# Kernel optimization log

Measured on AMD Instinct MI355X. Metric: run time of the kernel, lower is better.

## Reference

```python
import jax, jax.numpy as jnp
import numpy as np

HEADS, DH = 8, 64  # SelfAttention defaults: heads=8, dim_head=64


def _layernorm(x, g, b, eps=1e-5):
    mu = x.mean(-1, keepdims=True)
    var = ((x - mu) ** 2).mean(-1, keepdims=True)
    return (x - mu) / jnp.sqrt(var + eps) * g + b


def setup_inputs() -> dict:
    key = jax.random.key(0)
    ks = jax.random.split(key, 13)
    B, H, W, D, P = 1, 256, 256, 64, 128
    inner = HEADS * DH
    s = 0.05  # weight scale to keep logits in a sane range
    return {
        "x": jax.random.normal(ks[0], (B, H, W, D), jnp.float32),
        "pair_bias": jax.random.normal(ks[1], (B, W, W, P), jnp.float32),
        "Wq_w": jax.random.normal(ks[2], (D, inner), jnp.float32) * s,
        "Wkv_w": jax.random.normal(ks[3], (D, 2 * inner), jnp.float32) * s,
        "Wout_w": jax.random.normal(ks[4], (inner, D), jnp.float32) * s,
        "bout_w": jnp.zeros((D,), jnp.float32),
        "Wq_h": jax.random.normal(ks[5], (D, inner), jnp.float32) * s,
        "Wkv_h": jax.random.normal(ks[6], (D, 2 * inner), jnp.float32) * s,
        "Wout_h": jax.random.normal(ks[7], (inner, D), jnp.float32) * s,
        "bout_h": jnp.zeros((D,), jnp.float32),
        "pair_ln_g": jnp.ones((P,), jnp.float32),
        "pair_ln_b": jnp.zeros((P,), jnp.float32),
        "W_pair": jax.random.normal(ks[8], (P, HEADS), jnp.float32) * s,
    }


def _qkv(x2d, Wq, Wkv):
    # x2d: (N, L, D) -> q, k, v each (N, heads, L, dh)
    N, L, _ = x2d.shape
    q = (x2d @ Wq).reshape(N, L, HEADS, DH).transpose(0, 2, 1, 3)
    kv = (x2d @ Wkv).reshape(N, L, 2, HEADS, DH)
    k = kv[:, :, 0].transpose(0, 2, 1, 3)
    v = kv[:, :, 1].transpose(0, 2, 1, 3)
    return q, k, v


def reference(x, pair_bias, Wq_w, Wkv_w, Wout_w, bout_w,
              Wq_h, Wkv_h, Wout_h, bout_h, pair_ln_g, pair_ln_b, W_pair):
    B, H, W, D = x.shape  # B=1, H=n_seqs, W=length, D=dim
    scale = DH ** -0.5

    # ---- width attention: attend over seq dim H, batched per column (b*w) ----
    xw = jnp.transpose(x, (0, 2, 1, 3)).reshape(B * W, H, D)
    q, k, v = _qkv(xw, Wq_w, Wkv_w)
    dots = jnp.einsum('bhid,bhjd->bhij', q, k) * scale  # (B*W, heads, H, H)
    attn = jax.nn.softmax(dots, axis=-1)
    ow = jnp.einsum('bhij,bhjd->bhid', attn, v)
    ow = ow.transpose(0, 2, 1, 3).reshape(B * W, H, HEADS * DH)
    ow = ow @ Wout_w + bout_w
    w_out = ow.reshape(B, W, H, D).transpose(0, 2, 1, 3)  # (B, H, W, D)

    # ---- height attention: tied over seq dim (tie_attn_dim=H), pair bias ----
    xh = x.reshape(B * H, W, D)
    q, k, v = _qkv(xh, Wq_h, Wkv_h)           # (B*H, heads, W, dh)
    q = q.reshape(B, H, HEADS, W, DH)
    k = k.reshape(B, H, HEADS, W, DH)
    v = v.reshape(B, H, HEADS, W, DH)
    dots = jnp.einsum('brhid,brhjd->bhij', q, k) * scale * (H ** -0.5)  # (B, heads, W, W)
    pb = _layernorm(pair_bias, pair_ln_g, pair_ln_b) @ W_pair  # (B, W, W, heads)
    dots = dots + pb.transpose(0, 3, 1, 2)
    attn = jax.nn.softmax(dots, axis=-1)
    oh = jnp.einsum('bhij,brhjd->brhid', attn, v)  # (B, H, heads, W, dh)
    oh = oh.transpose(0, 1, 3, 2, 4).reshape(B, H, W, HEADS * DH)
    h_out = oh @ Wout_h + bout_h  # (B, H, W, D)

    return (w_out + h_out) * 0.5
```

## Files before the change

### kernel.cpp

```cpp
#include <hip/hip_runtime.h>
#include <hip/hip_bf16.h>

typedef __hip_bfloat16 bf16;
typedef __attribute__((ext_vector_type(8))) short bf16x8;
typedef __attribute__((ext_vector_type(4))) float f32x4;

#define MFMA16(a, b, c) __builtin_amdgcn_mfma_f32_16x16x32_bf16(a, b, c, 0, 0, 0)

#define HH 256
#define WW 256
#define NHEADS 8
#define NROWS 65536


__device__ __forceinline__ bf16x8 cvt8(const float* f) {
  bf16x8 r;
  bf16* h = (bf16*)&r;
#pragma unroll
  for (int i = 0; i < 8; i++) h[i] = __float2bfloat16(f[i]);
  return r;
}

__global__ void __launch_bounds__(256) k_xT2(const float* __restrict__ x,
                                             bf16* __restrict__ xh,
                                             bf16* __restrict__ xw) {
  const size_t idx = ((size_t)blockIdx.x * 256 + threadIdx.x) * 4;
  const float4 v = *(const float4*)(x + idx);
  bf16 tmp[4];
  tmp[0] = __float2bfloat16(v.x);
  tmp[1] = __float2bfloat16(v.y);
  tmp[2] = __float2bfloat16(v.z);
  tmp[3] = __float2bfloat16(v.w);
  *(uint2*)(xh + idx) = *(const uint2*)tmp;
  const int n = (int)(idx >> 6), d = (int)(idx & 63);
  const int h = n >> 8, w = n & 255;
  *(uint2*)(xw + (((size_t)((w << 8) | h)) << 6) + d) = *(const uint2*)tmp;
}

__global__ void __launch_bounds__(256) k_wt2(const float* __restrict__ Wq_w,
                                             const float* __restrict__ Wkv_w,
                                             const float* __restrict__ Wq_h,
                                             const float* __restrict__ Wkv_h,
                                             bf16* __restrict__ Wt_w,
                                             bf16* __restrict__ Wt_h) {
  int idx = blockIdx.x * 256 + threadIdx.x;
  const float* Wq = Wq_w;
  const float* Wkv = Wkv_w;
  bf16* Wt = Wt_w;
  if (idx >= 98304) { idx -= 98304; Wq = Wq_h; Wkv = Wkv_h; Wt = Wt_h; }
  const int k = idx / 1536, c = idx - k * 1536;
  const float val = (c < 512) ? Wq[k * 512 + c] : Wkv[k * 1024 + (c - 512)];
  Wt[(size_t)c * 64 + k] = __float2bfloat16(val);
}

__global__ void __launch_bounds__(256) k_wo(const float* __restrict__ Wout_w,
                                            const float* __restrict__ Wout_h,
                                            bf16* __restrict__ Wo_w,
                                            bf16* __restrict__ Wo_h) {
  int idx = blockIdx.x * 256 + threadIdx.x;
  const float* W = Wout_w;
  bf16* dst = Wo_w;
  if (idx >= 32768) { idx -= 32768; W = Wout_h; dst = Wo_h; }
  const int c = idx >> 9, d = idx & 511;
  dst[idx] = __float2bfloat16(W[d * 64 + c]);
}

__global__ void __launch_bounds__(256, 2)
k_width_fused(const bf16* __restrict__ xw, const bf16* __restrict__ Wt,
              bf16* __restrict__ Ow) {
  __shared__ __align__(16) char smem[53248];
  bf16* Ks = (bf16*)(smem + 20480);
  bf16* Vt = (bf16*)(smem + 36864);
  const int w = blockIdx.x, head = blockIdx.y;
  const int tid = threadIdx.x, lane = tid & 63, wv = tid >> 6;
  bf16* Qsc = (bf16*)(smem + wv * 5120);
  bf16* Ps  = (bf16*)(smem + wv * 5120);
  const int m16 = lane & 15, kq = lane >> 4;
  const int i0 = wv * 64;
  const bf16* xcol = xw + (size_t)w * 256 * 64;

  bf16x8 qf[4][2];
#pragma unroll
  for (int ch = 0; ch < 2; ch++) {
    bf16x8 af[2][2];
#pragma unroll
    for (int mt = 0; mt < 2; mt++) {
      const bf16* xr = xcol + (size_t)(i0 + ch * 32 + mt * 16 + m16) * 64 + kq * 8;
      af[mt][0] = *(const bf16x8*)xr;
      af[mt][1] = *(const bf16x8*)(xr + 32);
    }
#pragma unroll
    for (int nt = 0; nt < 4; nt++) {
      const bf16* wp = Wt + (size_t)(head * 64 + nt * 16 + m16) * 64 + kq * 8;
      const bf16x8 w0 = *(const bf16x8*)wp;
      const bf16x8 w1 = *(const bf16x8*)(wp + 32);
#pragma unroll
      for (int mt = 0; mt < 2; mt++) {
        f32x4 a = (f32x4){0.f, 0.f, 0.f, 0.f};
        a = MFMA16(af[mt][0], w0, a);
        a = MFMA16(af[mt][1], w1, a);
#pragma unroll
        for (int r = 0; r < 4; r++) {
          const int li = mt * 16 + kq * 4 + r;
          const int d = nt * 16 + m16;
          Qsc[li * 64 + (((d >> 3) ^ (li & 7)) << 3) + (d & 7)] = __float2bfloat16(a[r]);
        }
      }
    }
#pragma unroll
    for (int it = 0; it < 2; it++)
#pragma unroll
      for (int ks = 0; ks < 2; ks++) {
        const int li = it * 16 + m16;
        qf[ch * 2 + it][ks] =
            *(const bf16x8*)&Qsc[li * 64 + (((ks * 4 + kq) ^ (li & 7)) << 3)];
      }
  }

  f32x4 acc[4][4];
#pragma unroll
  for (int a = 0; a < 4; a++)
#pragma unroll
    for (int b = 0; b < 4; b++) acc[a][b] = (f32x4){0.f, 0.f, 0.f, 0.f};
  float rsum[4][4];
#pragma unroll
  for (int a = 0; a < 4; a++)
#pragma unroll
    for (int r = 0; r < 4; r++) rsum[a][r] = 0.f;

#pragma unroll 1
  for (int half = 0; half < 2; half++) {
    if (half) __syncthreads();
    bf16x8 afk[2][2];
#pragma unroll
    for (int mt = 0; mt < 2; mt++) {
      const int jrow = half * 128 + wv * 32 + mt * 16 + m16;
      const bf16* xr = xcol + (size_t)jrow * 64 + kq * 8;
      afk[mt][0] = *(const bf16x8*)xr;
      afk[mt][1] = *(const bf16x8*)(xr + 32);
    }
#pragma unroll
    for (int nt = 0; nt < 4; nt++) {
      const int d = nt * 16 + m16;
      {
        const bf16* wp = Wt + (size_t)(512 + head * 64 + d) * 64 + kq * 8;
        const bf16x8 w0 = *(const bf16x8*)wp;
        const bf16x8 w1 = *(const bf16x8*)(wp + 32);
#pragma unroll
        for (int mt = 0; mt < 2; mt++) {
          f32x4 a = (f32x4){0.f, 0.f, 0.f, 0.f};
          a = MFMA16(afk[mt][0], w0, a);
          a = MFMA16(afk[mt][1], w1, a);
#pragma unroll
          for (int r = 0; r < 4; r++) {
            const int jl = wv * 32 + mt * 16 + kq * 4 + r;
            Ks[jl * 64 + (((d >> 3) ^ (jl & 7)) << 3) + (d & 7)] = __float2bfloat16(a[r]);
          }
        }
      }
      {
        const bf16* wp = Wt + (size_t)(1024 + head * 64 + d) * 64 + kq * 8;
        const bf16x8 w0 = *(const bf16x8*)wp;
        const bf16x8 w1 = *(const bf16x8*)(wp + 32);
#pragma unroll
        for (int mt = 0; mt < 2; mt++) {
          f32x4 a = (f32x4){0.f, 0.f, 0.f, 0.f};
          a = MFMA16(afk[mt][0], w0, a);
          a = MFMA16(afk[mt][1], w1, a);
          const int jb = wv * 32 + mt * 16 + kq * 4;
          bf16 tmp[4];
#pragma unroll
          for (int r = 0; r < 4; r++) tmp[r] = __float2bfloat16(a[r]);
          *(uint2*)&Vt[d * 128 + (((jb >> 3) ^ (d & 7)) << 3) + (jb & 7)] =
              *(const uint2*)tmp;
        }
      }
    }
    __syncthreads();
#pragma unroll 1
    for (int jcl = 0; jcl < 4; jcl++) {
      bf16x8 kf[2][2];
#pragma unroll
      for (int jt = 0; jt < 2; jt++) {
        const int j = jcl * 32 + jt * 16 + m16;
#pragma unroll
        for (int ks = 0; ks < 2; ks++)
          kf[jt][ks] = *(const bf16x8*)&Ks[j * 64 + (((ks * 4 + kq) ^ (j & 7)) << 3)];
      }
#pragma unroll
      for (int it = 0; it < 4; it++)
#pragma unroll
        for (int jt = 0; jt < 2; jt++) {
          f32x4 s = (f32x4){0.f, 0.f, 0.f, 0.f};
          s = MFMA16(qf[it][0], kf[jt][0], s);
          s = MFMA16(qf[it][1], kf[jt][1], s);
#pragma unroll
          for (int r = 0; r < 4; r++) {
            float p = __expf(s[r] * 0.125f);
            rsum[it][r] += p;
            Ps[(it * 16 + kq * 4 + r) * 40 + jt * 16 + m16] = __float2bfloat16(p);
          }
        }
      bf16x8 pf[4], vf[4];
#pragma unroll
      for (int it = 0; it < 4; it++)
        pf[it] = *(const bf16x8*)&Ps[(it * 16 + m16) * 40 + kq * 8];
#pragma unroll
      for (int dt = 0; dt < 4; dt++)
        vf[dt] = *(const bf16x8*)&Vt[(dt * 16 + m16) * 128 +
                                     (((jcl * 4 + kq) ^ (m16 & 7)) << 3)];
#pragma unroll
      for (int it = 0; it < 4; it++)
#pragma unroll
        for (int dt = 0; dt < 4; dt++) acc[it][dt] = MFMA16(pf[it], vf[dt], acc[it][dt]);
    }
  }

#pragma unroll
  for (int it = 0; it < 4; it++)
#pragma unroll
    for (int r = 0; r < 4; r++) {
      float s = rsum[it][r];
      s += __shfl_xor(s, 1); s += __shfl_xor(s, 2);
      s += __shfl_xor(s, 4); s += __shfl_xor(s, 8);
      rsum[it][r] = 1.f / s;
    }
#pragma unroll
  for (int it = 0; it < 4; it++)
#pragma unroll
    for (int dt = 0; dt < 4; dt++)
#pragma unroll
      for (int r = 0; r < 4; r++) {
        const int i = i0 + it * 16 + kq * 4 + r;
        Ow[((size_t)(w * 256 + i)) * 512 + head * 64 + dt * 16 + m16] =
            __float2bfloat16(acc[it][dt][r] * rsum[it][r]);
      }
}

__global__ void __launch_bounds__(256, 2)
k_dots_f(const bf16* __restrict__ xh, const bf16* __restrict__ Wt, float* __restrict__ dp) {
  __shared__ __align__(16) bf16 Qs[64 * 72];
  __shared__ __align__(16) bf16 Ks[64 * 72];
  const int tile = blockIdx.x, head = blockIdx.y, rc = blockIdx.z;
  const int i0 = (tile >> 2) * 64, j0 = (tile & 3) * 64;
  const int tid = threadIdx.x, lane = tid & 63, wv = tid >> 6;
  const int m16 = lane & 15, kq = lane >> 4;
  float* slice = dp + (size_t)rc * 524288 + (size_t)head * 65536;

  const bf16* WtQ = Wt + (size_t)(head * 64) * 64 + kq * 8;
  const bf16* WtK = Wt + (size_t)(512 + head * 64) * 64 + kq * 8;

  f32x4 acc[4];
#pragma unroll
  for (int b = 0; b < 4; b++) acc[b] = (f32x4){0.f, 0.f, 0.f, 0.f};

  const int lrow = wv * 16 + kq * 4;

#pragma unroll 1
  for (int rr = 0; rr < 32; rr++) {
    const int rbase = (rc * 32 + rr) * 256;
    __syncthreads();
    {
      const bf16* xr = xh + (size_t)(rbase + i0 + wv * 16 + m16) * 64 + kq * 8;
      const bf16x8 qa0 = *(const bf16x8*)xr;
      const bf16x8 qa1 = *(const bf16x8*)(xr + 32);
      const bf16* yr = xh + (size_t)(rbase + j0 + wv * 16 + m16) * 64 + kq * 8;
      const bf16x8 ka0 = *(const bf16x8*)yr;
      const bf16x8 ka1 = *(const bf16x8*)(yr + 32);
#pragma unroll
      for (int nt = 0; nt < 4; nt++) {
        const bf16* wq = WtQ + (size_t)(nt * 16 + m16) * 64;
        f32x4 aq = (f32x4){0.f, 0.f, 0.f, 0.f};
        aq = MFMA16(qa0, *(const bf16x8*)wq, aq);
        aq = MFMA16(qa1, *(const bf16x8*)(wq + 32), aq);
        const bf16* wk = WtK + (size_t)(nt * 16 + m16) * 64;
        f32x4 ak = (f32x4){0.f, 0.f, 0.f, 0.f};
        ak = MFMA16(ka0, *(const bf16x8*)wk, ak);
        ak = MFMA16(ka1, *(const bf16x8*)(wk + 32), ak);
#pragma unroll
        for (int r = 0; r < 4; r++) {
          Qs[(lrow + r) * 72 + nt * 16 + m16] = __float2bfloat16(aq[r]);
          Ks[(lrow + r) * 72 + nt * 16 + m16] = __float2bfloat16(ak[r]);
        }
      }
    }
    __syncthreads();
#pragma unroll
    for (int ks = 0; ks < 2; ks++) {
      bf16x8 af = *(const bf16x8*)&Qs[(wv * 16 + m16) * 72 + ks * 32 + kq * 8];
      bf16x8 bfr[4];
#pragma unroll
      for (int jt = 0; jt < 4; jt++)
        bfr[jt] = *(const bf16x8*)&Ks[(jt * 16 + m16) * 72 + ks * 32 + kq * 8];
#pragma unroll
      for (int jt = 0; jt < 4; jt++) acc[jt] = MFMA16(af, bfr[jt], acc[jt]);
    }
  }
  const float sc = 1.f / 128.f;
#pragma unroll
  for (int jt = 0; jt < 4; jt++)
#pragma unroll
    for (int r = 0; r < 4; r++)
      slice[(size_t)(i0 + wv * 16 + kq * 4 + r) * 256 + j0 + jt * 16 + m16] = acc[jt][r] * sc;
}

__global__ void __launch_bounds__(256) k_pb(const float* __restrict__ pb,
                                            const float* __restrict__ g,
                                            const float* __restrict__ bb,
                                            const float* __restrict__ Wp,
                                            float* __restrict__ dots) {
  __shared__ float sn[4][128];
  const int tid = threadIdx.x, lane = tid & 63, wv = tid >> 6;
  const size_t ij = (size_t)blockIdx.x * 4 + wv;
  const float2 xv = *(const float2*)(pb + ij * 128 + lane * 2);

  float s = xv.x + xv.y;
#pragma unroll
  for (int o = 1; o < 64; o <<= 1) s += __shfl_xor(s, o);
  const float mu = s * (1.f / 128.f);
  const float d0 = xv.x - mu, d1 = xv.y - mu;
  float s2 = d0 * d0 + d1 * d1;
#pragma unroll
  for (int o = 1; o < 64; o <<= 1) s2 += __shfl_xor(s2, o);
  const float inv = rsqrtf(s2 * (1.f / 128.f) + 1e-5f);

  sn[wv][lane * 2 + 0] = d0 * inv * g[lane * 2 + 0] + bb[lane * 2 + 0];
  sn[wv][lane * 2 + 1] = d1 * inv * g[lane * 2 + 1] + bb[lane * 2 + 1];

  const int h = lane & 7, gp = lane >> 3;
  float a = 0.f;
#pragma unroll
  for (int p0 = 0; p0 < 16; p0++) {
    const int p = gp * 16 + p0;
    a += sn[wv][p] * Wp[p * 8 + h];
  }
  a += __shfl_xor(a, 8);
  a += __shfl_xor(a, 16);
  a += __shfl_xor(a, 32);
  if (lane < 8) dots[(size_t)h * 65536 + ij] += a;
}

__global__ void __launch_bounds__(256) k_softmax8(const float* __restrict__ dp,
                                                  bf16* __restrict__ P) {
  __shared__ float red[4];
  const int i = blockIdx.x, head = blockIdx.y, t = threadIdx.x;
  const size_t base = (size_t)head * 65536 + i * 256 + t;
  float lg = 0.f;
#pragma unroll
  for (int s = 0; s < 8; s++) lg += dp[(size_t)s * 524288 + base];
  const float e = __expf(lg);
  float s = e;
#pragma unroll
  for (int o = 1; o < 64; o <<= 1) s += __shfl_xor(s, o);
  if ((t & 63) == 0) red[t >> 6] = s;
  __syncthreads();
  const float S = red[0] + red[1] + red[2] + red[3];
  P[base] = __float2bfloat16(e / S);
}

__global__ void __launch_bounds__(256, 2)
k_h_pv_f(const bf16* __restrict__ P, const bf16* __restrict__ xh,
         const bf16* __restrict__ Wt, bf16* __restrict__ Oh) {
  __shared__ __align__(16) bf16 Vt[64 * 256];
  const int r = blockIdx.x, head = blockIdx.y;
  const int tid = threadIdx.x, lane = tid & 63, wv = tid >> 6;
  const int m16 = lane & 15, kq = lane >> 4;

  {
    const bf16* WtV = Wt + (size_t)(1024 + head * 64) * 64 + kq * 8;
#pragma unroll
    for (int mt = 0; mt < 4; mt++) {
      const int jb16 = wv * 64 + mt * 16;
      const bf16* xr = xh + (size_t)(r * 256 + jb16 + m16) * 64 + kq * 8;
      const bf16x8 a0 = *(const bf16x8*)xr;
      const bf16x8 a1 = *(const bf16x8*)(xr + 32);
#pragma unroll
      for (int nt = 0; nt < 4; nt++) {
        const int d = nt * 16 + m16;
        const bf16* wp = WtV + (size_t)(nt * 16 + m16) * 64;
        f32x4 a = (f32x4){0.f, 0.f, 0.f, 0.f};
        a = MFMA16(a0, *(const bf16x8*)wp, a);
        a = MFMA16(a1, *(const bf16x8*)(wp + 32), a);
        const int j = jb16 + kq * 4;
        bf16 tmp[4];
#pragma unroll
        for (int r2 = 0; r2 < 4; r2++) tmp[r2] = __float2bfloat16(a[r2]);
        *(uint2*)&Vt[d * 256 + (((j >> 3) ^ (d & 7)) << 3) + (j & 7)] = *(const uint2*)tmp;
      }
    }
  }

  const bf16* Pb = P + (size_t)head * 65536;
  const int i0 = wv * 64;
  auto loadP = [&](int ks, bf16x8 pf[4]) {
#pragma unroll
    for (int it = 0; it < 4; it++)
      pf[it] = *(const bf16x8*)(Pb + (size_t)(i0 + it * 16 + m16) * 256 + ks * 32 + kq * 8);
  };
  bf16x8 pcur[4];
  loadP(0, pcur);
  __syncthreads();

  f32x4 acc[4][4];
#pragma unroll
  for (int a = 0; a < 4; a++)
#pragma unroll
    for (int b = 0; b < 4; b++) acc[a][b] = (f32x4){0.f, 0.f, 0.f, 0.f};

#pragma unroll 1
  for (int ks = 0; ks < 8; ks++) {
    bf16x8 pnext[4];
    if (ks < 7) loadP(ks + 1, pnext);
    bf16x8 vf[4];
#pragma unroll
    for (int dt = 0; dt < 4; dt++)
      vf[dt] = *(const bf16x8*)&Vt[(dt * 16 + m16) * 256 + (((ks * 4 + kq) ^ (m16 & 7)) << 3)];
#pragma unroll
    for (int it = 0; it < 4; it++)
#pragma unroll
      for (int dt = 0; dt < 4; dt++) acc[it][dt] = MFMA16(pcur[it], vf[dt], acc[it][dt]);
    if (ks < 7) {
#pragma unroll
      for (int it = 0; it < 4; it++) pcur[it] = pnext[it];
    }
  }
#pragma unroll
  for (int it = 0; it < 4; it++)
#pragma unroll
    for (int dt = 0; dt < 4; dt++)
#pragma unroll
      for (int r2 = 0; r2 < 4; r2++) {
        const int i = i0 + it * 16 + kq * 4 + r2;
        Oh[((size_t)(r * 256 + i)) * 512 + head * 64 + dt * 16 + m16] =
            __float2bfloat16(acc[it][dt][r2]);
      }
}

__global__ void __launch_bounds__(256) k_outproj(const bf16* __restrict__ Ow,
                                                 const bf16* __restrict__ Oh,
                                                 const bf16* __restrict__ Wow,
                                                 const bf16* __restrict__ Woh,
                                                 const float* __restrict__ bw,
                                                 const float* __restrict__ bh,
                                                 float* __restrict__ out) {
  const int tid = threadIdx.x, lane = tid & 63, wv = tid >> 6;
  const int m16 = lane & 15, kq = lane >> 4;
  const int nA = blockIdx.x * 64 + wv * 16 + m16;
  const int wA = ((nA & 255) << 8) | (nA >> 8);

  const bf16* aw = Ow + (size_t)wA * 512 + kq * 8;
  const bf16* ah = Oh + (size_t)nA * 512 + kq * 8;

  f32x4 acc[4];
#pragma unroll
  for (int ct = 0; ct < 4; ct++) acc[ct] = (f32x4){0.f, 0.f, 0.f, 0.f};

#pragma unroll 1
  for (int kc = 0; kc < 16; kc++) {
    const bf16x8 afw = *(const bf16x8*)(aw + kc * 32);
    const bf16x8 afh = *(const bf16x8*)(ah + kc * 32);
#pragma unroll
    for (int ct = 0; ct < 4; ct++) {
      const bf16x8 bfw = *(const bf16x8*)(Wow + (size_t)(ct * 16 + m16) * 512 + kc * 32 + kq * 8);
      const bf16x8 bfh = *(const bf16x8*)(Woh + (size_t)(ct * 16 + m16) * 512 + kc * 32 + kq * 8);
      acc[ct] = MFMA16(afw, bfw, acc[ct]);
      acc[ct] = MFMA16(afh, bfh, acc[ct]);
    }
  }
  const int n0 = blockIdx.x * 64 + wv * 16 + kq * 4;
#pragma unroll
  for (int ct = 0; ct < 4; ct++) {
    const int c = ct * 16 + m16;
    const float bias = 0.5f * (bw[c] + bh[c]);
#pragma unroll
    for (int r = 0; r < 4; r++)
      out[(size_t)(n0 + r) * 64 + c] = 0.5f * acc[ct][r] + bias;
  }
}

extern "C" void kernel_launch(void* const* d_in, const int* in_sizes, int n_in,
                              void* d_out, int out_size, void* d_ws, size_t ws_size,
                              hipStream_t stream) {
  const float* x      = (const float*)d_in[0];
  const float* pair   = (const float*)d_in[1];
  const float* Wq_w   = (const float*)d_in[2];
  const float* Wkv_w  = (const float*)d_in[3];
  const float* Wout_w = (const float*)d_in[4];
  const float* bout_w = (const float*)d_in[5];
  const float* Wq_h   = (const float*)d_in[6];
  const float* Wkv_h  = (const float*)d_in[7];
  const float* Wout_h = (const float*)d_in[8];
  const float* bout_h = (const float*)d_in[9];
  const float* ln_g   = (const float*)d_in[10];
  const float* ln_b   = (const float*)d_in[11];
  const float* W_pair = (const float*)d_in[12];
  float* out = (float*)d_out;

  char* ws = (char*)d_ws;
  bf16* R0 = (bf16*)ws;
  bf16* xh = (bf16*)(ws + 67108864);
  bf16* xw = (bf16*)(ws + 67108864 + 8388608);
  bf16* R2 = (bf16*)(ws + 134217728);
  bf16* Wt_w = (bf16*)(ws + 201326592);
  bf16* Wt_h = (bf16*)(ws + 201326592 + 393216);
  bf16* P  = (bf16*)(ws + 201326592 + 786432);
  bf16* Wo_w = (bf16*)(ws + 201326592 + 1835008);
  bf16* Wo_h = Wo_w + 32768;
  float* dp = out;

  k_xT2<<<4096, 256, 0, stream>>>(x, xh, xw);
  k_wt2<<<768, 256, 0, stream>>>(Wq_w, Wkv_w, Wq_h, Wkv_h, Wt_w, Wt_h);
  k_wo<<<256, 256, 0, stream>>>(Wout_w, Wout_h, Wo_w, Wo_h);

  k_width_fused<<<dim3(WW, NHEADS), 256, 0, stream>>>(xw, Wt_w, R0);

  k_dots_f<<<dim3(16, NHEADS, 8), 256, 0, stream>>>(xh, Wt_h, dp);
  k_pb<<<65536 / 4, 256, 0, stream>>>(pair, ln_g, ln_b, W_pair, dp);
  k_softmax8<<<dim3(256, NHEADS), 256, 0, stream>>>(dp, P);
  k_h_pv_f<<<dim3(HH, NHEADS), 256, 0, stream>>>(P, xh, Wt_h, R2);

  k_outproj<<<1024, 256, 0, stream>>>(R0, R2, Wo_w, Wo_h, bout_w, bout_h, out);
}
```

Before: 447.1 us.

## Fold Q and K projections into per-head 64x64 bilinear matrix

Precomputes M = Wq_head · Wk_headᵀ for each head in a small kernel. Scores are then computed as (x·M)·xᵀ instead of projecting both Q and K. This removes the K projection and its shared-memory staging in both the width and height attention score kernels, and k_dots_f no longer needs block-wide barriers. In exchange, a second bf16 rounding of the fused matrix may change precision, and K fragments are now read directly from global memory.

```diff
diff --git a/kernel.cpp b/kernel.cpp
--- a/kernel.cpp
+++ b/kernel.cpp
@@ -65,12 +65,42 @@
   dst[idx] = __float2bfloat16(W[d * 64 + c]);
 }
 
+__global__ void __launch_bounds__(256) k_mb(const float* __restrict__ Wq_w,
+                                            const float* __restrict__ Wkv_w,
+                                            const float* __restrict__ Wq_h,
+                                            const float* __restrict__ Wkv_h,
+                                            bf16* __restrict__ Mb) {
+  __shared__ float Aq[64][64];
+  __shared__ float Ak[64][64];
+  const int phase = blockIdx.x >> 3, head = blockIdx.x & 7;
+  const float* Wq = phase ? Wq_h : Wq_w;
+  const float* Wkv = phase ? Wkv_h : Wkv_w;
+  const int t = threadIdx.x;
+#pragma unroll
+  for (int i = 0; i < 16; i++) {
+    const int idx = i * 256 + t;
+    const int r = idx >> 6, c = idx & 63;
+    Aq[r][c] = Wq[r * 512 + head * 64 + c];
+    Ak[r][c] = Wkv[r * 1024 + head * 64 + c];
+  }
+  __syncthreads();
+  bf16* dst = Mb + ((size_t)(phase * 8 + head)) * 4096;
+#pragma unroll
+  for (int i = 0; i < 16; i++) {
+    const int idx = i * 256 + t;
+    const int d2 = idx >> 6, d1 = idx & 63;
+    float s = 0.f;
+#pragma unroll
+    for (int dh = 0; dh < 64; dh++) s += Aq[d1][dh] * Ak[d2][dh];
+    dst[idx] = __float2bfloat16(s);
+  }
+}
+
 __global__ void __launch_bounds__(256, 2)
 k_width_fused(const bf16* __restrict__ xw, const bf16* __restrict__ Wt,
-              bf16* __restrict__ Ow) {
-  __shared__ __align__(16) char smem[53248];
-  bf16* Ks = (bf16*)(smem + 20480);
-  bf16* Vt = (bf16*)(smem + 36864);
+              const bf16* __restrict__ Mb, bf16* __restrict__ Ow) {
+  __shared__ __align__(16) char smem[36864];
+  bf16* Vt = (bf16*)(smem + 20480);
   const int w = blockIdx.x, head = blockIdx.y;
   const int tid = threadIdx.x, lane = tid & 63, wv = tid >> 6;
   bf16* Qsc = (bf16*)(smem + wv * 5120);
@@ -78,8 +108,9 @@
   const int m16 = lane & 15, kq = lane >> 4;
   const int i0 = wv * 64;
   const bf16* xcol = xw + (size_t)w * 256 * 64;
-
-  bf16x8 qf[4][2];
+  const bf16* Mh = Mb + (size_t)head * 4096;
+
+  bf16x8 yf[4][2];
 #pragma unroll
   for (int ch = 0; ch < 2; ch++) {
     bf16x8 af[2][2];
@@ -91,7 +122,7 @@
     }
 #pragma unroll
     for (int nt = 0; nt < 4; nt++) {
-      const bf16* wp = Wt + (size_t)(head * 64 + nt * 16 + m16) * 64 + kq * 8;
+      const bf16* wp = Mh + (size_t)(nt * 16 + m16) * 64 + kq * 8;
       const bf16x8 w0 = *(const bf16x8*)wp;
       const bf16x8 w1 = *(const bf16x8*)(wp + 32);
 #pragma unroll
@@ -112,7 +143,7 @@
 #pragma unroll
       for (int ks = 0; ks < 2; ks++) {
         const int li = it * 16 + m16;
-        qf[ch * 2 + it][ks] =
+        yf[ch * 2 + it][ks] =
             *(const bf16x8*)&Qsc[li * 64 + (((ks * 4 + kq) ^ (li & 7)) << 3)];
       }
   }
@@ -142,38 +173,20 @@
 #pragma unroll
     for (int nt = 0; nt < 4; nt++) {
       const int d = nt * 16 + m16;
-      {
-        const bf16* wp = Wt + (size_t)(512 + head * 64 + d) * 64 + kq * 8;
-        const bf16x8 w0 = *(const bf16x8*)wp;
-        const bf16x8 w1 = *(const bf16x8*)(wp + 32);
-#pragma unroll
-        for (int mt = 0; mt < 2; mt++) {
-          f32x4 a = (f32x4){0.f, 0.f, 0.f, 0.f};
-          a = MFMA16(afk[mt][0], w0, a);
-          a = MFMA16(afk[mt][1], w1, a);
-#pragma unroll
-          for (int r = 0; r < 4; r++) {
-            const int jl = wv * 32 + mt * 16 + kq * 4 + r;
-            Ks[jl * 64 + (((d >> 3) ^ (jl & 7)) << 3) + (d & 7)] = __float2bfloat16(a[r]);
-          }
-        }
-      }
-      {
-        const bf16* wp = Wt + (size_t)(1024 + head * 64 + d) * 64 + kq * 8;
-        const bf16x8 w0 = *(const bf16x8*)wp;
-        const bf16x8 w1 = *(const bf16x8*)(wp + 32);
-#pragma unroll
-        for (int mt = 0; mt < 2; mt++) {
-          f32x4 a = (f32x4){0.f, 0.f, 0.f, 0.f};
-          a = MFMA16(afk[mt][0], w0, a);
-          a = MFMA16(afk[mt][1], w1, a);
-          const int jb = wv * 32 + mt * 16 + kq * 4;
-          bf16 tmp[4];
-#pragma unroll
-          for (int r = 0; r < 4; r++) tmp[r] = __float2bfloat16(a[r]);
-          *(uint2*)&Vt[d * 128 + (((jb >> 3) ^ (d & 7)) << 3) + (jb & 7)] =
-              *(const uint2*)tmp;
-        }
+      const bf16* wp = Wt + (size_t)(1024 + head * 64 + d) * 64 + kq * 8;
+      const bf16x8 w0 = *(const bf16x8*)wp;
+      const bf16x8 w1 = *(const bf16x8*)(wp + 32);
+#pragma unroll
+      for (int mt = 0; mt < 2; mt++) {
+        f32x4 a = (f32x4){0.f, 0.f, 0.f, 0.f};
+        a = MFMA16(afk[mt][0], w0, a);
+        a = MFMA16(afk[mt][1], w1, a);
+        const int jb = wv * 32 + mt * 16 + kq * 4;
+        bf16 tmp[4];
+#pragma unroll
+        for (int r = 0; r < 4; r++) tmp[r] = __float2bfloat16(a[r]);
+        *(uint2*)&Vt[d * 128 + (((jb >> 3) ^ (d & 7)) << 3) + (jb & 7)] =
+            *(const uint2*)tmp;
       }
     }
     __syncthreads();
@@ -182,18 +195,18 @@
       bf16x8 kf[2][2];
 #pragma unroll
       for (int jt = 0; jt < 2; jt++) {
-        const int j = jcl * 32 + jt * 16 + m16;
-#pragma unroll
-        for (int ks = 0; ks < 2; ks++)
-          kf[jt][ks] = *(const bf16x8*)&Ks[j * 64 + (((ks * 4 + kq) ^ (j & 7)) << 3)];
+        const int j = half * 128 + jcl * 32 + jt * 16 + m16;
+        const bf16* xr = xcol + (size_t)j * 64 + kq * 8;
+        kf[jt][0] = *(const bf16x8*)xr;
+        kf[jt][1] = *(const bf16x8*)(xr + 32);
       }
 #pragma unroll
       for (int it = 0; it < 4; it++)
 #pragma unroll
         for (int jt = 0; jt < 2; jt++) {
           f32x4 s = (f32x4){0.f, 0.f, 0.f, 0.f};
-          s = MFMA16(qf[it][0], kf[jt][0], s);
-          s = MFMA16(qf[it][1], kf[jt][1], s);
+          s = MFMA16(yf[it][0], kf[jt][0], s);
+          s = MFMA16(yf[it][1], kf[jt][1], s);
 #pragma unroll
           for (int r = 0; r < 4; r++) {
             float p = __expf(s[r] * 0.125f);
@@ -237,61 +250,56 @@
       }
 }
 
-__global__ void __launch_bounds__(256, 2)
-k_dots_f(const bf16* __restrict__ xh, const bf16* __restrict__ Wt, float* __restrict__ dp) {
-  __shared__ __align__(16) bf16 Qs[64 * 72];
-  __shared__ __align__(16) bf16 Ks[64 * 72];
+__global__ void __launch_bounds__(256)
+k_dots_f(const bf16* __restrict__ xh, const bf16* __restrict__ Mb, float* __restrict__ dp) {
+  __shared__ __align__(16) bf16 Ysc[4][16 * 72];
   const int tile = blockIdx.x, head = blockIdx.y, rc = blockIdx.z;
   const int i0 = (tile >> 2) * 64, j0 = (tile & 3) * 64;
   const int tid = threadIdx.x, lane = tid & 63, wv = tid >> 6;
   const int m16 = lane & 15, kq = lane >> 4;
   float* slice = dp + (size_t)rc * 524288 + (size_t)head * 65536;
 
-  const bf16* WtQ = Wt + (size_t)(head * 64) * 64 + kq * 8;
-  const bf16* WtK = Wt + (size_t)(512 + head * 64) * 64 + kq * 8;
+  const bf16* Mh = Mb + (size_t)(8 + head) * 4096;
+  bf16x8 mf[4][2];
+#pragma unroll
+  for (int nt = 0; nt < 4; nt++) {
+    const bf16* wp = Mh + (size_t)(nt * 16 + m16) * 64 + kq * 8;
+    mf[nt][0] = *(const bf16x8*)wp;
+    mf[nt][1] = *(const bf16x8*)(wp + 32);
+  }
 
   f32x4 acc[4];
 #pragma unroll
   for (int b = 0; b < 4; b++) acc[b] = (f32x4){0.f, 0.f, 0.f, 0.f};
 
-  const int lrow = wv * 16 + kq * 4;
+  const int lrow = kq * 4;
+  bf16* ysc = Ysc[wv];
 
 #pragma unroll 1
   for (int rr = 0; rr < 32; rr++) {
     const int rbase = (rc * 32 + rr) * 256;
-    __syncthreads();
     {
       const bf16* xr = xh + (size_t)(rbase + i0 + wv * 16 + m16) * 64 + kq * 8;
       const bf16x8 qa0 = *(const bf16x8*)xr;
       const bf16x8 qa1 = *(const bf16x8*)(xr + 32);
-      const bf16* yr = xh + (size_t)(rbase + j0 + wv * 16 + m16) * 64 + kq * 8;
-      const bf16x8 ka0 = *(const bf16x8*)yr;
-      const bf16x8 ka1 = *(const bf16x8*)(yr + 32);
 #pragma unroll
       for (int nt = 0; nt < 4; nt++) {
-        const bf16* wq = WtQ + (size_t)(nt * 16 + m16) * 64;
         f32x4 aq = (f32x4){0.f, 0.f, 0.f, 0.f};
-        aq = MFMA16(qa0, *(const bf16x8*)wq, aq);
-        aq = MFMA16(qa1, *(const bf16x8*)(wq + 32), aq);
-        const bf16* wk = WtK + (size_t)(nt * 16 + m16) * 64;
-        f32x4 ak = (f32x4){0.f, 0.f, 0.f, 0.f};
-        ak = MFMA16(ka0, *(const bf16x8*)wk, ak);
-        ak = MFMA16(ka1, *(const bf16x8*)(wk + 32), ak);
-#pragma unroll
-        for (int r = 0; r < 4; r++) {
-          Qs[(lrow + r) * 72 + nt * 16 + m16] = __float2bfloat16(aq[r]);
-          Ks[(lrow + r) * 72 + nt * 16 + m16] = __float2bfloat16(ak[r]);
-        }
-      }
-    }
-    __syncthreads();
+        aq = MFMA16(qa0, mf[nt][0], aq);
+        aq = MFMA16(qa1, mf[nt][1], aq);
+#pragma unroll
+        for (int r = 0; r < 4; r++)
+          ysc[(lrow + r) * 72 + nt * 16 + m16] = __float2bfloat16(aq[r]);
+      }
+    }
 #pragma unroll
     for (int ks = 0; ks < 2; ks++) {
-      bf16x8 af = *(const bf16x8*)&Qs[(wv * 16 + m16) * 72 + ks * 32 + kq * 8];
+      bf16x8 af = *(const bf16x8*)&ysc[m16 * 72 + ks * 32 + kq * 8];
       bf16x8 bfr[4];
 #pragma unroll
       for (int jt = 0; jt < 4; jt++)
-        bfr[jt] = *(const bf16x8*)&Ks[(jt * 16 + m16) * 72 + ks * 32 + kq * 8];
+        bfr[jt] = *(const bf16x8*)(xh + (size_t)(rbase + j0 + jt * 16 + m16) * 64 +
+                                   ks * 32 + kq * 8);
 #pragma unroll
       for (int jt = 0; jt < 4; jt++) acc[jt] = MFMA16(af, bfr[jt], acc[jt]);
     }
@@ -506,15 +514,17 @@
   bf16* P  = (bf16*)(ws + 201326592 + 786432);
   bf16* Wo_w = (bf16*)(ws + 201326592 + 1835008);
   bf16* Wo_h = Wo_w + 32768;
+  bf16* Mb = (bf16*)(ws + 201326592 + 1966080);
   float* dp = out;
 
   k_xT2<<<4096, 256, 0, stream>>>(x, xh, xw);
   k_wt2<<<768, 256, 0, stream>>>(Wq_w, Wkv_w, Wq_h, Wkv_h, Wt_w, Wt_h);
   k_wo<<<256, 256, 0, stream>>>(Wout_w, Wout_h, Wo_w, Wo_h);
-
-  k_width_fused<<<dim3(WW, NHEADS), 256, 0, stream>>>(xw, Wt_w, R0);
-
-  k_dots_f<<<dim3(16, NHEADS, 8), 256, 0, stream>>>(xh, Wt_h, dp);
+  k_mb<<<16, 256, 0, stream>>>(Wq_w, Wkv_w, Wq_h, Wkv_h, Mb);
+
+  k_width_fused<<<dim3(WW, NHEADS), 256, 0, stream>>>(xw, Wt_w, Mb, R0);
+
+  k_dots_f<<<dim3(16, NHEADS, 8), 256, 0, stream>>>(xh, Mb, dp);
   k_pb<<<65536 / 4, 256, 0, stream>>>(pair, ln_g, ln_b, W_pair, dp);
   k_softmax8<<<dim3(256, NHEADS), 256, 0, stream>>>(dp, P);
   k_h_pv_f<<<dim3(HH, NHEADS), 256, 0, stream>>>(P, xh, Wt_h, R2);
```

New measurement: 631.8 us. +41.3%, slower.
